# Performance work log

Measured on AMD Instinct MI355X. Metric: run time of the kernel, lower is better.

The kernel has to match this reference:

```python
import jax, jax.numpy as jnp
import numpy as np

N, DEG = 50000, 16
E = N * DEG
IN_DIM, OUT_DIM, HEADS = 256, 64, 4
SLOPE = 0.01  # torch F.leaky_relu default negative_slope


def setup_inputs() -> dict:
    key = jax.random.key(0)
    k1, k2, k3, k4, k5 = jax.random.split(key, 5)
    h = jax.random.normal(k1, (N, IN_DIM), dtype=jnp.float32)
    W = jax.random.normal(k2, (HEADS, IN_DIM, OUT_DIM), dtype=jnp.float32) * 0.05
    a_src = jax.random.normal(k3, (HEADS, OUT_DIM), dtype=jnp.float32) * 0.05
    a_dst = jax.random.normal(k4, (HEADS, OUT_DIM), dtype=jnp.float32) * 0.05
    src = jax.random.randint(k5, (E,), 0, N, dtype=jnp.int32)
    # every node receives exactly DEG messages (non-empty mailboxes, as in g.pull)
    dst = jnp.repeat(jnp.arange(N, dtype=jnp.int32), DEG)
    return {"h": h, "W": W, "a_src": a_src, "a_dst": a_dst, "src": src, "dst": dst}


def reference(h, W, a_src, a_dst, src, dst):
    # per-head projection: z[n,h,d]
    z = jnp.einsum('ni,hid->nhd', h, W)
    # concat(z_src,z_dst)@attn_fc == z_src.a_src + z_dst.a_dst (per head)
    es = jnp.einsum('nhd,hd->nh', z, a_src)  # [N,H]
    ed = jnp.einsum('nhd,hd->nh', z, a_dst)  # [N,H]
    e = es[src] + ed[dst]                    # [E,H]
    e = jnp.where(e >= 0, e, SLOPE * e)      # leaky_relu
    # segment softmax over incoming edges of each dst node
    m = jax.ops.segment_max(e, dst, num_segments=N)          # [N,H]
    ex = jnp.exp(e - m[dst])                                  # [E,H]
    denom = jax.ops.segment_sum(ex, dst, num_segments=N)     # [N,H]
    alpha = ex / denom[dst]                                   # [E,H]
    # weighted segment-sum of source features
    msg = alpha[:, :, None] * z[src]                          # [E,H,D]
    out = jax.ops.segment_sum(msg, dst, num_segments=N)      # [N,H,D]
    return out.reshape(N, HEADS * OUT_DIM)  # merge='cat'
```

## Files before the change

### kernel.cpp

```cpp
#include <hip/hip_runtime.h>
#include <hip/hip_bf16.h>

#define N_NODES 50000
#define DEG 16
#define IN_DIM 256
#define OUT_DIM 64
#define HEADS 4
#define C_DIM 256
#define SLOPE 0.01f

typedef __attribute__((ext_vector_type(8))) short short8;
typedef __attribute__((ext_vector_type(4))) float f32x4;

static __device__ __forceinline__ unsigned short f2bf(float f) {
    union { float f; unsigned int i; } v; v.f = f;
    unsigned int u = v.i;
    return (unsigned short)((u + 0x7fffu + ((u >> 16) & 1u)) >> 16);
}
static __device__ __forceinline__ unsigned int cvt_pk_bf16(float lo, float hi) {
    unsigned int w;
    asm("v_cvt_pk_bf16_f32 %0, %1, %2" : "=v"(w) : "v"(lo), "v"(hi));
    return w;
}
static __device__ __forceinline__ short8 pack8(float4 a0, float4 a1) {
    union { unsigned int w[4]; short8 s; } u;
    u.w[0] = cvt_pk_bf16(a0.x, a0.y);
    u.w[1] = cvt_pk_bf16(a0.z, a0.w);
    u.w[2] = cvt_pk_bf16(a1.x, a1.y);
    u.w[3] = cvt_pk_bf16(a1.z, a1.w);
    return u.s;
}
static __device__ __forceinline__ float i8f(unsigned int word, int b) {
    return (float)(int)(signed char)((word >> (8 * b)) & 0xffu);
}

#define GLOAD_LDS16(gsrc, ldst)                                                      \
    __builtin_amdgcn_global_load_lds(                                                \
        (const __attribute__((address_space(1))) unsigned int*)(gsrc),               \
        (__attribute__((address_space(3))) unsigned int*)(ldst), 16, 0, 0)

__global__ __launch_bounds__(256) void k_prep(const float* __restrict__ W,
                                              unsigned char* __restrict__ Bp) {
    const int c = blockIdx.x;
    const int k = threadIdx.x;
    const int hh = c >> 6, d = c & 63;
    const unsigned short v = f2bf(W[hh * (IN_DIM * OUT_DIM) + k * OUT_DIM + d]);
    const int s = k >> 6, kk = k & 63;
    int off = ((kk >> 5) << 14) + c * 64 + (((kk >> 3) & 3) << 4) + ((kk & 7) << 1);
    off ^= (c & 7) << 4;
    *(unsigned short*)(Bp + (size_t)s * 32768 + off) = v;
}

__global__ __launch_bounds__(256) void k_proj(const float* __restrict__ h,
                                              const unsigned char* __restrict__ Bp,
                                              const float* __restrict__ a_src,
                                              const float* __restrict__ a_dst,
                                              unsigned char* __restrict__ qz,
                                              float* __restrict__ scale,
                                              float* __restrict__ es,
                                              float* __restrict__ ed) {
    __shared__ unsigned char Bs[32768];
    const int tid  = threadIdx.x;
    const int lane = tid & 63;
    const int wave = tid >> 6;
    const int wb   = blockIdx.x * 64 + wave * 16;
    const int n    = lane & 15;
    const int g    = lane >> 4;

    int arow = wb + n; if (arow >= N_NODES) arow = N_NODES - 1;
    const float* hrow = h + (size_t)arow * IN_DIM;

    const int lbase = (n * 64 + g * 16) ^ ((n & 7) << 4);

    f32x4 acc[16];
    #pragma unroll
    for (int ct = 0; ct < 16; ct++) acc[ct] = (f32x4){0.f, 0.f, 0.f, 0.f};

    {
        const unsigned char* bs = Bp + wave * 1024 + lane * 16;
        #pragma unroll
        for (int i = 0; i < 8; i++)
            GLOAD_LDS16(bs + i * 4096, &Bs[i * 4096 + wave * 1024]);
    }
    short8 af0, af1;
    {
        float4 a0 = *(const float4*)(hrow + g * 8);
        float4 a1 = *(const float4*)(hrow + g * 8 + 4);
        float4 a2 = *(const float4*)(hrow + 32 + g * 8);
        float4 a3 = *(const float4*)(hrow + 32 + g * 8 + 4);
        af0 = pack8(a0, a1);
        af1 = pack8(a2, a3);
    }

    #pragma unroll
    for (int s = 0; s < 4; s++) {
        __syncthreads();
        float4 na0, na1, na2, na3;
        if (s < 3) {
            na0 = *(const float4*)(hrow + (s + 1) * 64 + g * 8);
            na1 = *(const float4*)(hrow + (s + 1) * 64 + g * 8 + 4);
            na2 = *(const float4*)(hrow + (s + 1) * 64 + 32 + g * 8);
            na3 = *(const float4*)(hrow + (s + 1) * 64 + 32 + g * 8 + 4);
        }
        #pragma unroll
        for (int ct = 0; ct < 16; ct++) {
            union { uint4 u; short8 s8; } b0, b1;
            b0.u = *(const uint4*)(&Bs[ct * 1024 + lbase]);
            b1.u = *(const uint4*)(&Bs[16384 + ct * 1024 + lbase]);
            acc[ct] = __builtin_amdgcn_mfma_f32_16x16x32_bf16(af0, b0.s8, acc[ct], 0, 0, 0);
            acc[ct] = __builtin_amdgcn_mfma_f32_16x16x32_bf16(af1, b1.s8, acc[ct], 0, 0, 0);
        }
        if (s < 3) {
            af0 = pack8(na0, na1);
            af1 = pack8(na2, na3);
            __syncthreads();
            const unsigned char* bs = Bp + (size_t)(s + 1) * 32768 + wave * 1024 + lane * 16;
            #pragma unroll
            for (int i = 0; i < 8; i++)
                GLOAD_LDS16(bs + i * 4096, &Bs[i * 4096 + wave * 1024]);
        }
    }

    __syncthreads();
    {
        unsigned char* my = &Bs[wave * 8192];
        float rmax[4];
        #pragma unroll
        for (int r = 0; r < 4; r++) {
            float mx = 0.f;
            #pragma unroll
            for (int ct = 0; ct < 16; ct++) mx = fmaxf(mx, fabsf(acc[ct][r]));
            #pragma unroll
            for (int o = 1; o < 16; o <<= 1) mx = fmaxf(mx, __shfl_xor(mx, o, 64));
            rmax[r] = fmaxf(mx, 1e-30f);
        }
        if (n < 4) {
            const int m = wb + g * 4 + n;
            if (m < N_NODES) scale[m] = rmax[n] * (1.0f / 127.0f);
        }
        #pragma unroll
        for (int r = 0; r < 4; r++) {
            const float inv = 127.0f / rmax[r];
            const int row = g * 4 + r;
            #pragma unroll
            for (int ct = 0; ct < 16; ct++) {
                const int qv = (int)rintf(acc[ct][r] * inv);
                my[row * 256 + ct * 16 + n] = (unsigned char)qv;
            }
        }
        #pragma unroll
        for (int i = 0; i < 4; i++) {
            const int chunk = i * 64 + lane;
            const int row = chunk >> 4;
            const int m = wb + row;
            const uint4 v = *(const uint4*)&my[chunk * 16];
            if (m < N_NODES) *(uint4*)(qz + (size_t)m * C_DIM + (chunk & 15) * 16) = v;
        }
    }

    float keep_s = 0.f, keep_d = 0.f;
    #pragma unroll
    for (int hh = 0; hh < 4; hh++) {
        #pragma unroll
        for (int r = 0; r < 4; r++) {
            float vs = 0.f, vd = 0.f;
            #pragma unroll
            for (int q = 0; q < 4; q++) {
                const int ct = hh * 4 + q;
                const int c  = ct * 16 + n;
                vs = fmaf(acc[ct][r], a_src[c], vs);
                vd = fmaf(acc[ct][r], a_dst[c], vd);
            }
            #pragma unroll
            for (int o = 1; o < 16; o <<= 1) {
                vs += __shfl_xor(vs, o, 64);
                vd += __shfl_xor(vd, o, 64);
            }
            if (n == (hh << 2 | r)) { keep_s = vs; keep_d = vd; }
        }
    }
    {
        const int m = wb + g * 4 + (n & 3);
        const int hh = n >> 2;
        if (m < N_NODES) {
            es[m * 4 + hh] = keep_s;
            ed[m * 4 + hh] = keep_d;
        }
    }
}

__global__ __launch_bounds__(256) void k_attn(const unsigned char* __restrict__ qz,
                                              const float* __restrict__ scale,
                                              const float* __restrict__ es,
                                              const float* __restrict__ ed,
                                              const int* __restrict__ src,
                                              float* __restrict__ out) {
    const int lane = threadIdx.x & 63;
    const int wave = threadIdx.x >> 6;
    const int base = blockIdx.x * 8 + wave * 2;
    const int j16 = lane & 15;
    const int h4 = lane >> 4;
    const int half = lane >> 5;
    const int q    = lane & 31;
    const int headq = q >> 3;

    const int s0 = src[base * DEG + j16];
    const int s1 = src[(base + 1) * DEG + j16];

    uint2 rows0[8], rows1[8];
    #pragma unroll
    for (int t = 0; t < 8; t++) {
        const int sj = __shfl(s0, 2 * t + half, 64);
        rows0[t] = *(const uint2*)(qz + (size_t)sj * C_DIM + q * 8);
    }
    #pragma unroll
    for (int t = 0; t < 8; t++) {
        const int sj = __shfl(s1, 2 * t + half, 64);
        rows1[t] = *(const uint2*)(qz + (size_t)sj * C_DIM + q * 8);
    }

    const float sc0 = scale[s0];
    const float sc1 = scale[s1];

    float e0 = es[s0 * 4 + h4] + ed[base * 4 + h4];
    e0 = (e0 >= 0.f) ? e0 : SLOPE * e0;
    float e1 = es[s1 * 4 + h4] + ed[(base + 1) * 4 + h4];
    e1 = (e1 >= 0.f) ? e1 : SLOPE * e1;
    float m0 = e0, m1 = e1;
    #pragma unroll
    for (int o = 1; o < 16; o <<= 1) {
        m0 = fmaxf(m0, __shfl_xor(m0, o, 64));
        m1 = fmaxf(m1, __shfl_xor(m1, o, 64));
    }
    const float ex0 = __expf(e0 - m0);
    const float ex1 = __expf(e1 - m1);
    float sum0 = ex0, sum1 = ex1;
    #pragma unroll
    for (int o = 1; o < 16; o <<= 1) {
        sum0 += __shfl_xor(sum0, o, 64);
        sum1 += __shfl_xor(sum1, o, 64);
    }
    const float beta0 = (ex0 / sum0) * sc0;
    const float beta1 = (ex1 / sum1) * sc1;

    float acc0[8], acc1[8];
    #pragma unroll
    for (int c = 0; c < 8; c++) { acc0[c] = 0.f; acc1[c] = 0.f; }
    #pragma unroll
    for (int t = 0; t < 8; t++) {
        const float al0 = __shfl(beta0, headq * 16 + 2 * t + half, 64);
        const uint2 v0 = rows0[t];
        #pragma unroll
        for (int b = 0; b < 4; b++) {
            acc0[b]     = fmaf(al0, i8f(v0.x, b), acc0[b]);
            acc0[b + 4] = fmaf(al0, i8f(v0.y, b), acc0[b + 4]);
        }
        const float al1 = __shfl(beta1, headq * 16 + 2 * t + half, 64);
        const uint2 v1 = rows1[t];
        #pragma unroll
        for (int b = 0; b < 4; b++) {
            acc1[b]     = fmaf(al1, i8f(v1.x, b), acc1[b]);
            acc1[b + 4] = fmaf(al1, i8f(v1.y, b), acc1[b + 4]);
        }
    }
    #pragma unroll
    for (int c = 0; c < 8; c++) {
        acc0[c] += __shfl_xor(acc0[c], 32, 64);
        acc1[c] += __shfl_xor(acc1[c], 32, 64);
    }

    const float4 w0 = half ? make_float4(acc0[4], acc0[5], acc0[6], acc0[7])
                           : make_float4(acc0[0], acc0[1], acc0[2], acc0[3]);
    *(float4*)(out + (size_t)base * C_DIM + q * 8 + half * 4) = w0;
    const float4 w1 = half ? make_float4(acc1[4], acc1[5], acc1[6], acc1[7])
                           : make_float4(acc1[0], acc1[1], acc1[2], acc1[3]);
    *(float4*)(out + (size_t)(base + 1) * C_DIM + q * 8 + half * 4) = w1;
}

extern "C" void kernel_launch(void* const* d_in, const int* in_sizes, int n_in,
                              void* d_out, int out_size, void* d_ws, size_t ws_size,
                              hipStream_t stream) {
    const float* h     = (const float*)d_in[0];
    const float* W     = (const float*)d_in[1];
    const float* a_src = (const float*)d_in[2];
    const float* a_dst = (const float*)d_in[3];
    const int*   src   = (const int*)d_in[4];

    unsigned char* qz = (unsigned char*)d_ws;
    float* scale = (float*)((char*)d_ws + (size_t)N_NODES * C_DIM);
    float* es    = scale + N_NODES;
    float* ed    = es + (size_t)N_NODES * HEADS;
    unsigned char* Bp = (unsigned char*)(ed + (size_t)N_NODES * HEADS);
    float* out = (float*)d_out;

    hipLaunchKernelGGL(k_prep, dim3(C_DIM),               dim3(IN_DIM), 0, stream, W, Bp);
    hipLaunchKernelGGL(k_proj, dim3((N_NODES + 63) / 64), dim3(256),    0, stream,
                       h, Bp, a_src, a_dst, qz, scale, es, ed);
    hipLaunchKernelGGL(k_attn, dim3(N_NODES / 8),         dim3(256),    0, stream,
                       qz, scale, es, ed, src, out);
}
```

Measured before the change: 71.60 us.

## Fold attention vectors into weights and give each wave two row tiles

A new prep kernel precomputes W·a_src and W·a_dst as extra bf16 weight columns. k_proj then gets es/ed from one extra MFMA tile instead of running shuffle reductions over the accumulators. k_proj also moves to 128-thread blocks where each wave computes 32 rows, reusing each LDS B-fragment load for two MFMAs. This doubles accumulator registers per wave, which risks lower occupancy, adds a kernel launch, and computes es/ed from bf16-rounded folded weights.

After: 74.28 us. 1.04x slower.

```diff
diff --git a/kernel.cpp b/kernel.cpp
--- a/kernel.cpp
+++ b/kernel.cpp
@@ -51,10 +51,36 @@
     *(unsigned short*)(Bp + (size_t)s * 32768 + off) = v;
 }
 
-__global__ __launch_bounds__(256) void k_proj(const float* __restrict__ h,
+__global__ __launch_bounds__(256) void k_prep2(const float* __restrict__ W,
+                                               const float* __restrict__ a_src,
+                                               const float* __restrict__ a_dst,
+                                               unsigned short* __restrict__ Bx) {
+    const int k = blockIdx.x;
+    const int t = threadIdx.x;
+    const int hh = t >> 6, d = t & 63;
+    const float w = W[hh * (IN_DIM * OUT_DIM) + k * OUT_DIM + d];
+    float ps = w * a_src[hh * OUT_DIM + d];
+    float pd = w * a_dst[hh * OUT_DIM + d];
+    #pragma unroll
+    for (int o = 1; o < 64; o <<= 1) {
+        ps += __shfl_xor(ps, o, 64);
+        pd += __shfl_xor(pd, o, 64);
+    }
+    const int s = k >> 6, kh = (k >> 5) & 1, g = (k >> 3) & 3, j = k & 7;
+    const int base = (s * 2 + kh) * 512 + g * 128 + j;
+    if (d == 0) {
+        Bx[base + hh * 8]       = f2bf(ps);
+        Bx[base + (4 + hh) * 8] = f2bf(pd);
+    }
+    if (d == 1) {
+        Bx[base + (8 + hh) * 8]  = 0;
+        Bx[base + (12 + hh) * 8] = 0;
+    }
+}
+
+__global__ __launch_bounds__(128) void k_proj(const float* __restrict__ h,
                                               const unsigned char* __restrict__ Bp,
-                                              const float* __restrict__ a_src,
-                                              const float* __restrict__ a_dst,
+                                              const unsigned short* __restrict__ Bx,
                                               unsigned char* __restrict__ qz,
                                               float* __restrict__ scale,
                                               float* __restrict__ es,
@@ -63,93 +89,129 @@
     const int tid  = threadIdx.x;
     const int lane = tid & 63;
     const int wave = tid >> 6;
-    const int wb   = blockIdx.x * 64 + wave * 16;
+    const int wb   = blockIdx.x * 64 + wave * 32;
     const int n    = lane & 15;
     const int g    = lane >> 4;
 
-    int arow = wb + n; if (arow >= N_NODES) arow = N_NODES - 1;
-    const float* hrow = h + (size_t)arow * IN_DIM;
+    int ar0 = wb + n;      if (ar0 >= N_NODES) ar0 = N_NODES - 1;
+    int ar1 = wb + 16 + n; if (ar1 >= N_NODES) ar1 = N_NODES - 1;
+    const float* hr0 = h + (size_t)ar0 * IN_DIM;
+    const float* hr1 = h + (size_t)ar1 * IN_DIM;
 
     const int lbase = (n * 64 + g * 16) ^ ((n & 7) << 4);
-
-    f32x4 acc[16];
-    #pragma unroll
-    for (int ct = 0; ct < 16; ct++) acc[ct] = (f32x4){0.f, 0.f, 0.f, 0.f};
+    const unsigned short* bxl = Bx + g * 128 + n * 8;
+
+    f32x4 acc0[16], acc1[16];
+    #pragma unroll
+    for (int ct = 0; ct < 16; ct++) {
+        acc0[ct] = (f32x4){0.f, 0.f, 0.f, 0.f};
+        acc1[ct] = (f32x4){0.f, 0.f, 0.f, 0.f};
+    }
+    f32x4 acce0 = (f32x4){0.f, 0.f, 0.f, 0.f};
+    f32x4 acce1 = (f32x4){0.f, 0.f, 0.f, 0.f};
 
     {
         const unsigned char* bs = Bp + wave * 1024 + lane * 16;
         #pragma unroll
-        for (int i = 0; i < 8; i++)
-            GLOAD_LDS16(bs + i * 4096, &Bs[i * 4096 + wave * 1024]);
-    }
-    short8 af0, af1;
+        for (int i = 0; i < 16; i++)
+            GLOAD_LDS16(bs + i * 2048, &Bs[i * 2048 + wave * 1024]);
+    }
+    short8 af0, af1, ag0, ag1;
     {
-        float4 a0 = *(const float4*)(hrow + g * 8);
-        float4 a1 = *(const float4*)(hrow + g * 8 + 4);
-        float4 a2 = *(const float4*)(hrow + 32 + g * 8);
-        float4 a3 = *(const float4*)(hrow + 32 + g * 8 + 4);
-        af0 = pack8(a0, a1);
-        af1 = pack8(a2, a3);
-    }
+        af0 = pack8(*(const float4*)(hr0 + g * 8), *(const float4*)(hr0 + g * 8 + 4));
+        af1 = pack8(*(const float4*)(hr0 + 32 + g * 8), *(const float4*)(hr0 + 32 + g * 8 + 4));
+        ag0 = pack8(*(const float4*)(hr1 + g * 8), *(const float4*)(hr1 + g * 8 + 4));
+        ag1 = pack8(*(const float4*)(hr1 + 32 + g * 8), *(const float4*)(hr1 + 32 + g * 8 + 4));
+    }
+    uint4 bx0 = *(const uint4*)(bxl);
+    uint4 bx1 = *(const uint4*)(bxl + 512);
 
     #pragma unroll
     for (int s = 0; s < 4; s++) {
         __syncthreads();
-        float4 na0, na1, na2, na3;
+        float4 na0, na1, na2, na3, nb0, nb1, nb2, nb3;
+        uint4 bxn0, bxn1;
         if (s < 3) {
-            na0 = *(const float4*)(hrow + (s + 1) * 64 + g * 8);
-            na1 = *(const float4*)(hrow + (s + 1) * 64 + g * 8 + 4);
-            na2 = *(const float4*)(hrow + (s + 1) * 64 + 32 + g * 8);
-            na3 = *(const float4*)(hrow + (s + 1) * 64 + 32 + g * 8 + 4);
+            na0 = *(const float4*)(hr0 + (s + 1) * 64 + g * 8);
+            na1 = *(const float4*)(hr0 + (s + 1) * 64 + g * 8 + 4);
+            na2 = *(const float4*)(hr0 + (s + 1) * 64 + 32 + g * 8);
+            na3 = *(const float4*)(hr0 + (s + 1) * 64 + 32 + g * 8 + 4);
+            nb0 = *(const float4*)(hr1 + (s + 1) * 64 + g * 8);
+            nb1 = *(const float4*)(hr1 + (s + 1) * 64 + g * 8 + 4);
+            nb2 = *(const float4*)(hr1 + (s + 1) * 64 + 32 + g * 8);
+            nb3 = *(const float4*)(hr1 + (s + 1) * 64 + 32 + g * 8 + 4);
+            bxn0 = *(const uint4*)(bxl + (s + 1) * 1024);
+            bxn1 = *(const uint4*)(bxl + (s + 1) * 1024 + 512);
         }
         #pragma unroll
         for (int ct = 0; ct < 16; ct++) {
             union { uint4 u; short8 s8; } b0, b1;
             b0.u = *(const uint4*)(&Bs[ct * 1024 + lbase]);
             b1.u = *(const uint4*)(&Bs[16384 + ct * 1024 + lbase]);
-            acc[ct] = __builtin_amdgcn_mfma_f32_16x16x32_bf16(af0, b0.s8, acc[ct], 0, 0, 0);
-            acc[ct] = __builtin_amdgcn_mfma_f32_16x16x32_bf16(af1, b1.s8, acc[ct], 0, 0, 0);
+            acc0[ct] = __builtin_amdgcn_mfma_f32_16x16x32_bf16(af0, b0.s8, acc0[ct], 0, 0, 0);
+            acc0[ct] = __builtin_amdgcn_mfma_f32_16x16x32_bf16(af1, b1.s8, acc0[ct], 0, 0, 0);
+            acc1[ct] = __builtin_amdgcn_mfma_f32_16x16x32_bf16(ag0, b0.s8, acc1[ct], 0, 0, 0);
+            acc1[ct] = __builtin_amdgcn_mfma_f32_16x16x32_bf16(ag1, b1.s8, acc1[ct], 0, 0, 0);
+        }
+        {
+            union { uint4 u; short8 s8; } e0, e1;
+            e0.u = bx0; e1.u = bx1;
+            acce0 = __builtin_amdgcn_mfma_f32_16x16x32_bf16(af0, e0.s8, acce0, 0, 0, 0);
+            acce0 = __builtin_amdgcn_mfma_f32_16x16x32_bf16(af1, e1.s8, acce0, 0, 0, 0);
+            acce1 = __builtin_amdgcn_mfma_f32_16x16x32_bf16(ag0, e0.s8, acce1, 0, 0, 0);
+            acce1 = __builtin_amdgcn_mfma_f32_16x16x32_bf16(ag1, e1.s8, acce1, 0, 0, 0);
         }
         if (s < 3) {
-            af0 = pack8(na0, na1);
-            af1 = pack8(na2, na3);
+            af0 = pack8(na0, na1); af1 = pack8(na2, na3);
+            ag0 = pack8(nb0, nb1); ag1 = pack8(nb2, nb3);
+            bx0 = bxn0; bx1 = bxn1;
             __syncthreads();
             const unsigned char* bs = Bp + (size_t)(s + 1) * 32768 + wave * 1024 + lane * 16;
             #pragma unroll
-            for (int i = 0; i < 8; i++)
-                GLOAD_LDS16(bs + i * 4096, &Bs[i * 4096 + wave * 1024]);
+            for (int i = 0; i < 16; i++)
+                GLOAD_LDS16(bs + i * 2048, &Bs[i * 2048 + wave * 1024]);
         }
     }
 
     __syncthreads();
     {
-        unsigned char* my = &Bs[wave * 8192];
-        float rmax[4];
+        unsigned char* my = &Bs[wave * 16384];
+        float rmax0[4], rmax1[4];
         #pragma unroll
         for (int r = 0; r < 4; r++) {
-            float mx = 0.f;
+            float m0 = 0.f, m1 = 0.f;
             #pragma unroll
-            for (int ct = 0; ct < 16; ct++) mx = fmaxf(mx, fabsf(acc[ct][r]));
+            for (int ct = 0; ct < 16; ct++) {
+                m0 = fmaxf(m0, fabsf(acc0[ct][r]));
+                m1 = fmaxf(m1, fabsf(acc1[ct][r]));
+            }
             #pragma unroll
-            for (int o = 1; o < 16; o <<= 1) mx = fmaxf(mx, __shfl_xor(mx, o, 64));
-            rmax[r] = fmaxf(mx, 1e-30f);
+            for (int o = 1; o < 16; o <<= 1) {
+                m0 = fmaxf(m0, __shfl_xor(m0, o, 64));
+                m1 = fmaxf(m1, __shfl_xor(m1, o, 64));
+            }
+            rmax0[r] = fmaxf(m0, 1e-30f);
+            rmax1[r] = fmaxf(m1, 1e-30f);
         }
         if (n < 4) {
             const int m = wb + g * 4 + n;
-            if (m < N_NODES) scale[m] = rmax[n] * (1.0f / 127.0f);
+            if (m < N_NODES) scale[m] = rmax0[n] * (1.0f / 127.0f);
+            const int m2 = wb + 16 + g * 4 + n;
+            if (m2 < N_NODES) scale[m2] = rmax1[n] * (1.0f / 127.0f);
         }
         #pragma unroll
         for (int r = 0; r < 4; r++) {
-            const float inv = 127.0f / rmax[r];
-            const int row = g * 4 + r;
+            const float inv0 = 127.0f / rmax0[r];
+            const float inv1 = 127.0f / rmax1[r];
+            const int row0 = g * 4 + r, row1 = 16 + g * 4 + r;
             #pragma unroll
             for (int ct = 0; ct < 16; ct++) {
-                const int qv = (int)rintf(acc[ct][r] * inv);
-                my[row * 256 + ct * 16 + n] = (unsigned char)qv;
+                my[row0 * 256 + ct * 16 + n] = (unsigned char)(int)rintf(acc0[ct][r] * inv0);
+                my[row1 * 256 + ct * 16 + n] = (unsigned char)(int)rintf(acc1[ct][r] * inv1);
             }
         }
         #pragma unroll
-        for (int i = 0; i < 4; i++) {
+        for (int i = 0; i < 8; i++) {
             const int chunk = i * 64 + lane;
             const int row = chunk >> 4;
             const int m = wb + row;
@@ -158,33 +220,17 @@
         }
     }
 
-    float keep_s = 0.f, keep_d = 0.f;
-    #pragma unroll
-    for (int hh = 0; hh < 4; hh++) {
-        #pragma unroll
-        for (int r = 0; r < 4; r++) {
-            float vs = 0.f, vd = 0.f;
-            #pragma unroll
-            for (int q = 0; q < 4; q++) {
-                const int ct = hh * 4 + q;
-                const int c  = ct * 16 + n;
-                vs = fmaf(acc[ct][r], a_src[c], vs);
-                vd = fmaf(acc[ct][r], a_dst[c], vd);
-            }
-            #pragma unroll
-            for (int o = 1; o < 16; o <<= 1) {
-                vs += __shfl_xor(vs, o, 64);
-                vd += __shfl_xor(vd, o, 64);
-            }
-            if (n == (hh << 2 | r)) { keep_s = vs; keep_d = vd; }
-        }
-    }
-    {
-        const int m = wb + g * 4 + (n & 3);
-        const int hh = n >> 2;
+    #pragma unroll
+    for (int r = 0; r < 4; r++) {
+        const int m = wb + g * 4 + r;
         if (m < N_NODES) {
-            es[m * 4 + hh] = keep_s;
-            ed[m * 4 + hh] = keep_d;
+            if (n < 4)      es[m * 4 + n]       = acce0[r];
+            else if (n < 8) ed[m * 4 + (n - 4)] = acce0[r];
+        }
+        const int m2 = wb + 16 + g * 4 + r;
+        if (m2 < N_NODES) {
+            if (n < 4)      es[m2 * 4 + n]       = acce1[r];
+            else if (n < 8) ed[m2 * 4 + (n - 4)] = acce1[r];
         }
     }
 }
@@ -291,11 +337,13 @@
     float* es    = scale + N_NODES;
     float* ed    = es + (size_t)N_NODES * HEADS;
     unsigned char* Bp = (unsigned char*)(ed + (size_t)N_NODES * HEADS);
+    unsigned short* Bx = (unsigned short*)(Bp + 4 * 32768);
     float* out = (float*)d_out;
 
-    hipLaunchKernelGGL(k_prep, dim3(C_DIM),               dim3(IN_DIM), 0, stream, W, Bp);
-    hipLaunchKernelGGL(k_proj, dim3((N_NODES + 63) / 64), dim3(256),    0, stream,
-                       h, Bp, a_src, a_dst, qz, scale, es, ed);
-    hipLaunchKernelGGL(k_attn, dim3(N_NODES / 8),         dim3(256),    0, stream,
+    hipLaunchKernelGGL(k_prep,  dim3(C_DIM), dim3(IN_DIM), 0, stream, W, Bp);
+    hipLaunchKernelGGL(k_prep2, dim3(C_DIM), dim3(IN_DIM), 0, stream, W, a_src, a_dst, Bx);
+    hipLaunchKernelGGL(k_proj,  dim3((N_NODES + 63) / 64), dim3(128), 0, stream,
+                       h, Bp, Bx, qz, scale, es, ed);
+    hipLaunchKernelGGL(k_attn,  dim3(N_NODES / 8),         dim3(256), 0, stream,
                        qz, scale, es, ed, src, out);
 }
```
